# Optimization experiments

Measured on AMD Instinct MI355X. Metric: run time of the kernel, lower is better.

The kernel has to match this reference:

```python
import jax, jax.numpy as jnp
import numpy as np

HID = 4096
NH = 32
NKV = 8
HD = 128
ROPE_BASE = 1000000.0
EPS = 1e-6
Q_SIZE = NH * HD      # 4096
KV_SIZE = NKV * HD    # 1024


def rms_norm(x, w):
    # x: [..., HD]
    var = jnp.mean(x * x, axis=-1, keepdims=True)
    return x * jax.lax.rsqrt(var + EPS) * w


def apply_rope(x, cos, sin):
    # x: [T, H, HD], cos/sin: [T, 1, HD//2]; neox-style rotate-half
    x1, x2 = jnp.split(x, 2, axis=-1)
    return jnp.concatenate([x1 * cos - x2 * sin, x2 * cos + x1 * sin], axis=-1)


def setup_inputs() -> dict:
    key = jax.random.key(0)
    ks = jax.random.split(key, 8)
    T = 4096
    inp = {
        "positions": jnp.arange(T, dtype=jnp.int32),
        "hidden_states": jax.random.normal(ks[0], (T, HID), dtype=jnp.float32),
        "ctx_len": 3072,
        "w_qkv": jax.random.normal(ks[1], (HID, Q_SIZE + 2 * KV_SIZE), dtype=jnp.float32) * 0.02,
        "b_qkv": jax.random.normal(ks[2], (Q_SIZE + 2 * KV_SIZE,), dtype=jnp.float32) * 0.02,
        "q_norm_w": 1.0 + 0.02 * jax.random.normal(ks[3], (HD,), dtype=jnp.float32),
        "k_norm_w": 1.0 + 0.02 * jax.random.normal(ks[4], (HD,), dtype=jnp.float32),
        "w_o": jax.random.normal(ks[5], (Q_SIZE, HID), dtype=jnp.float32) * 0.02,
    }
    return inp


def reference(positions, hidden_states, ctx_len, w_qkv, b_qkv, q_norm_w, k_norm_w, w_o):
    T = hidden_states.shape[0]
    noise_len = T - ctx_len

    qkv = hidden_states @ w_qkv + b_qkv                     # [T, 6144]
    q = qkv[:, :Q_SIZE].reshape(T, NH, HD)
    k = qkv[:, Q_SIZE:Q_SIZE + KV_SIZE].reshape(T, NKV, HD)
    v = qkv[:, Q_SIZE + KV_SIZE:].reshape(T, NKV, HD)

    # per-head RMSNorm on q and k
    q = rms_norm(q, q_norm_w)
    k = rms_norm(k, k_norm_w)

    # RoPE (neox style, full rotary dim)
    half = HD // 2
    inv_freq = 1.0 / (ROPE_BASE ** (jnp.arange(half, dtype=jnp.float32) / half))
    freqs = positions.astype(jnp.float32)[:, None] * inv_freq[None, :]   # [T, half]
    cos = jnp.cos(freqs)[:, None, :]
    sin = jnp.sin(freqs)[:, None, :]
    q = apply_rope(q, cos, sin)
    k = apply_rope(k, cos, sin)

    # Q from noise positions only; K/V from full sequence (non-causal)
    qn = q[ctx_len:]                                        # [N, NH, HD]
    g = NH // NKV
    qn = qn.reshape(noise_len, NKV, g, HD)                  # [N, kv, g, HD]
    scale = HD ** -0.5

    # scores: [kv, g, N, T] in fp32 (faithful to fp32 softmax)
    scores = jnp.einsum("nkgd,tkd->kgnt", qn, k) * scale
    probs = jax.nn.softmax(scores.astype(jnp.float32), axis=-1).astype(v.dtype)
    out = jnp.einsum("kgnt,tkd->nkgd", probs, v)            # [N, kv, g, HD]
    out = out.reshape(noise_len, NH * HD)
    return out @ w_o                                        # [N, HID]
```

## Files before the change

### kernel.cpp

```cpp
#include <hip/hip_runtime.h>
#include <stdint.h>

#define NH 32
#define NKV 8
#define HD 128
#define HID 4096
#define NQKV 6144

typedef __attribute__((ext_vector_type(8))) __bf16 bf16x8;
typedef __attribute__((ext_vector_type(4))) float f32x4;
typedef __attribute__((ext_vector_type(4))) float float4v;
typedef __attribute__((ext_vector_type(8))) unsigned short ushort8v;
typedef __attribute__((ext_vector_type(4))) unsigned short ushort4v;
typedef __attribute__((ext_vector_type(2))) unsigned short ushort2v;

__device__ __forceinline__ unsigned short f2bf(float f) {
  union { float f; unsigned u; } x; x.f = f;
  unsigned r = x.u + 0x7fffu + ((x.u >> 16) & 1u);
  return (unsigned short)(r >> 16);
}

__device__ __forceinline__ void gld16(const void* g, void* l) {
  __builtin_amdgcn_global_load_lds(
      (const __attribute__((address_space(1))) unsigned int*)g,
      (__attribute__((address_space(3))) unsigned int*)l, 16, 0, 0);
}

__device__ __forceinline__ f32x4 mfma16(bf16x8 a, bf16x8 b, f32x4 c) {
  return __builtin_amdgcn_mfma_f32_16x16x32_bf16(a, b, c, 0, 0, 0);
}

__global__ void ropetab(const int* __restrict__ pos, float* __restrict__ cosT,
                        float* __restrict__ sinT) {
  const int t = blockIdx.x, f = threadIdx.x;
  const double inv = exp(-0.2158673524681918 * (double)f);
  const double arg = (double)pos[t] * inv;
  cosT[t * 64 + f] = (float)cos(arg);
  sinT[t * 64 + f] = (float)sin(arg);
}

__global__ void convbf(const float* __restrict__ src, unsigned short* __restrict__ dst,
                       long n4) {
  long i = (long)blockIdx.x * blockDim.x + threadIdx.x;
  const long stride = (long)gridDim.x * blockDim.x;
  for (; i < n4; i += stride) {
    float4v v = *(const float4v*)(src + i * 4);
    ushort4v o;
    o.x = f2bf(v.x); o.y = f2bf(v.y); o.z = f2bf(v.z); o.w = f2bf(v.w);
    *(ushort4v*)(dst + i * 4) = o;
  }
}

__global__ __launch_bounds__(256) void wtrans(const float* __restrict__ W,
                                              unsigned short* __restrict__ Wt,
                                              int K, int N) {
  __shared__ float tile[64][65];
  const int k0 = blockIdx.y * 64, n0 = blockIdx.x * 64;
  const int tid = threadIdx.x;
  const int rk = tid >> 4, cn = (tid & 15) * 4;
#pragma unroll
  for (int rr = 0; rr < 64; rr += 16) {
    float4v v = *(const float4v*)(W + (long)(k0 + rk + rr) * N + n0 + cn);
    tile[rk + rr][cn] = v.x; tile[rk + rr][cn + 1] = v.y;
    tile[rk + rr][cn + 2] = v.z; tile[rk + rr][cn + 3] = v.w;
  }
  __syncthreads();
  const int rn = tid >> 3, ck = (tid & 7) * 8;
#pragma unroll
  for (int rr = 0; rr < 64; rr += 32) {
    ushort8v o;
#pragma unroll
    for (int j = 0; j < 8; ++j) o[j] = f2bf(tile[ck + j][rn + rr]);
    *(ushort8v*)(Wt + (long)(n0 + rn + rr) * K + k0 + ck) = o;
  }
}

__global__ __launch_bounds__(256) void vtrans(const float* __restrict__ qkv,
                                              unsigned short* __restrict__ Vt, int T) {
  __shared__ float tile[64][65];
  const int kvh = blockIdx.z;
  const int t0 = blockIdx.x * 64, d0 = blockIdx.y * 64;
  const int tid = threadIdx.x;
  const int rt = tid >> 4, cd = (tid & 15) * 4;
#pragma unroll
  for (int rr = 0; rr < 64; rr += 16) {
    float4v v = *(const float4v*)(qkv + (long)(t0 + rt + rr) * NQKV + 5120 + kvh * 128 + d0 + cd);
    tile[rt + rr][cd] = v.x; tile[rt + rr][cd + 1] = v.y;
    tile[rt + rr][cd + 2] = v.z; tile[rt + rr][cd + 3] = v.w;
  }
  __syncthreads();
  const int rd = tid >> 3, ct = (tid & 7) * 8;
#pragma unroll
  for (int rr = 0; rr < 64; rr += 32) {
    ushort8v o;
#pragma unroll
    for (int j = 0; j < 8; ++j) o[j] = f2bf(tile[ct + j][rd + rr]);
    *(ushort8v*)(Vt + ((long)kvh * 128 + d0 + rd + rr) * T + t0 + ct) = o;
  }
}

__global__ __launch_bounds__(256) void norm_rope(
    const float* __restrict__ qkv, const float* __restrict__ qw,
    const float* __restrict__ kw, const float* __restrict__ cosT,
    const float* __restrict__ sinT, unsigned short* __restrict__ Qo,
    unsigned short* __restrict__ Ko, int T, int ctx, int noise) {
  const int t = blockIdx.x;
  __shared__ float cs[64], sn[64];
  const int tid = threadIdx.x;
  if (tid < 64) { cs[tid] = cosT[t * 64 + tid]; sn[tid] = sinT[t * 64 + tid]; }
  __syncthreads();
  const int wid = tid >> 6, lane = tid & 63;
  const float* row = qkv + (long)t * NQKV;
  const bool isNoise = (t >= ctx);
  for (int sl = wid; sl < 40; sl += 4) {
    if (sl < 32 && !isNoise) continue;
    const float* x = row + sl * 128;
    float v0 = x[lane * 2], v1 = x[lane * 2 + 1];
    float ss = v0 * v0 + v1 * v1;
#pragma unroll
    for (int off = 32; off >= 1; off >>= 1) ss += __shfl_xor(ss, off);
    const float rinv = rsqrtf(ss * (1.f / 128.f) + 1e-6f);
    const float* w = (sl < 32) ? qw : kw;
    v0 *= rinv * w[lane * 2];
    v1 *= rinv * w[lane * 2 + 1];
    const float p0 = __shfl_xor(v0, 32);
    const float p1 = __shfl_xor(v1, 32);
    const int f0 = (lane * 2) & 63, f1 = (lane * 2 + 1) & 63;
    float o0, o1;
    if (lane < 32) { o0 = v0 * cs[f0] - p0 * sn[f0]; o1 = v1 * cs[f1] - p1 * sn[f1]; }
    else           { o0 = v0 * cs[f0] + p0 * sn[f0]; o1 = v1 * cs[f1] + p1 * sn[f1]; }
    ushort2v o; o.x = f2bf(o0); o.y = f2bf(o1);
    if (sl < 32)
      *(ushort2v*)(Qo + ((long)sl * noise + (t - ctx)) * 128 + lane * 2) = o;
    else
      *(ushort2v*)(Ko + ((long)(sl - 32) * T + t) * 128 + lane * 2) = o;
  }
}

__global__ __launch_bounds__(256) void gemm_bt(
    const unsigned short* __restrict__ A, const unsigned short* __restrict__ Bt,
    float* __restrict__ C, const float* __restrict__ bias, int M, int N, int K) {
  __shared__ unsigned short As[128 * 32];
  __shared__ unsigned short Bs[128 * 32];
  const int tid = threadIdx.x;
  const int wid = tid >> 6, lane = tid & 63;
  const int lr = lane & 15, lg = lane >> 4;
  const long bm = (long)blockIdx.y * 128;
  const long bn = (long)blockIdx.x * 128;
  const int wm = (wid >> 1) * 64;
  const int wn = (wid & 1) * 64;
  const int nz = gridDim.z;
  const int kLen = K / nz;
  const int kOff = blockIdx.z * kLen;
  f32x4 acc[4][4] = {};
  for (int k0 = kOff; k0 < kOff + kLen; k0 += 32) {
#pragma unroll
    for (int c = 0; c < 2; ++c) {
      const int q = c * 4 + wid;
      const int idx = q * 64 + lane;
      const int r = idx >> 2;
      const int ce = (idx & 3) * 8;
      gld16(A + (bm + r) * (long)K + k0 + ce, As + q * 512);
      gld16(Bt + (bn + r) * (long)K + k0 + ce, Bs + q * 512);
    }
    __syncthreads();
    bf16x8 af[4], bfv[4];
#pragma unroll
    for (int i = 0; i < 4; ++i) {
      af[i]  = *(const bf16x8*)(As + (wm + i * 16 + lr) * 32 + lg * 8);
      bfv[i] = *(const bf16x8*)(Bs + (wn + i * 16 + lr) * 32 + lg * 8);
    }
#pragma unroll
    for (int i = 0; i < 4; ++i)
#pragma unroll
      for (int j = 0; j < 4; ++j)
        acc[i][j] = mfma16(af[i], bfv[j], acc[i][j]);
    __syncthreads();
  }
  if (nz == 1) {
#pragma unroll
    for (int i = 0; i < 4; ++i) {
#pragma unroll
      for (int j = 0; j < 4; ++j) {
        const long row = bm + wm + i * 16 + lg * 4;
        const long col = bn + wn + j * 16 + lr;
        const float b = bias ? bias[col] : 0.f;
#pragma unroll
        for (int r = 0; r < 4; ++r)
          C[(row + r) * (long)N + col] = acc[i][j][r] + b;
      }
    }
  } else {
#pragma unroll
    for (int i = 0; i < 4; ++i) {
#pragma unroll
      for (int j = 0; j < 4; ++j) {
        const long row = bm + wm + i * 16 + lg * 4;
        const long col = bn + wn + j * 16 + lr;
#pragma unroll
        for (int r = 0; r < 4; ++r)
          atomicAdd(&C[(row + r) * (long)N + col], acc[i][j][r]);
      }
    }
  }
}

__global__ __launch_bounds__(256) void attn_kernel(
    const unsigned short* __restrict__ Q, const unsigned short* __restrict__ Kb,
    const unsigned short* __restrict__ Vt, unsigned short* __restrict__ Oout,
    int noise, int T, float scale) {
  __shared__ unsigned short Ks[64 * 128];
  __shared__ unsigned short Vs[128 * 64];
  __shared__ unsigned short Ps[4 * 16 * 64];
  const int h = blockIdx.y;
  const int kvh = h >> 2;
  const int tid = threadIdx.x, wid = tid >> 6, lane = tid & 63;
  const int lr = lane & 15, lg = lane >> 4;
  const unsigned short* qb = Q + ((long)h * noise + blockIdx.x * 64 + wid * 16 + lr) * 128;
  bf16x8 qf[4];
#pragma unroll
  for (int kc = 0; kc < 4; ++kc) qf[kc] = *(const bf16x8*)(qb + kc * 32 + lg * 8);
  const unsigned short* kbase = Kb + (long)kvh * T * 128;
  const unsigned short* vbase = Vt + (long)kvh * 128 * T;
  f32x4 accO[8] = {};
  float m_r[4], l_r[4];
#pragma unroll
  for (int r = 0; r < 4; ++r) { m_r[r] = -1e30f; l_r[r] = 0.f; }
  unsigned short* pw = Ps + wid * 1024;
  const int sw = (lr & 7) << 3;
  for (int t0 = 0; t0 < T; t0 += 64) {
#pragma unroll
    for (int c = 0; c < 4; ++c) {
      const int q = c * 4 + wid;
      const int idx = q * 64 + lane;
      const int kgi = (idx & ~7) | ((idx ^ (idx >> 4)) & 7);
      gld16(kbase + (long)t0 * 128 + (long)kgi * 8, Ks + q * 512);
      const int d = idx >> 3;
      const int cg = (idx ^ d) & 7;
      gld16(vbase + (long)d * T + t0 + cg * 8, Vs + q * 512);
    }
    __syncthreads();
    f32x4 s[4] = {};
    __builtin_amdgcn_s_setprio(1);
#pragma unroll
    for (int kc = 0; kc < 4; ++kc)
#pragma unroll
      for (int nt = 0; nt < 4; ++nt) {
        bf16x8 kf = *(const bf16x8*)(Ks + (nt * 16 + lr) * 128 + (((kc * 32) + lg * 8) ^ sw));
        s[nt] = mfma16(qf[kc], kf, s[nt]);
      }
    __builtin_amdgcn_s_setprio(0);
#pragma unroll
    for (int nt = 0; nt < 4; ++nt)
#pragma unroll
      for (int r = 0; r < 4; ++r) s[nt][r] *= scale;
    float mt[4], rs[4];
#pragma unroll
    for (int r = 0; r < 4; ++r)
      mt[r] = fmaxf(fmaxf(s[0][r], s[1][r]), fmaxf(s[2][r], s[3][r]));
#pragma unroll
    for (int off = 8; off >= 1; off >>= 1)
#pragma unroll
      for (int r = 0; r < 4; ++r) mt[r] = fmaxf(mt[r], __shfl_xor(mt[r], off));
    float corr[4];
#pragma unroll
    for (int r = 0; r < 4; ++r) {
      const float mn = fmaxf(m_r[r], mt[r]);
      corr[r] = __expf(m_r[r] - mn);
      m_r[r] = mn;
      rs[r] = 0.f;
    }
#pragma unroll
    for (int nt = 0; nt < 4; ++nt)
#pragma unroll
      for (int r = 0; r < 4; ++r) {
        const float p = __expf(s[nt][r] - m_r[r]);
        s[nt][r] = p;
        rs[r] += p;
      }
#pragma unroll
    for (int off = 8; off >= 1; off >>= 1)
#pragma unroll
      for (int r = 0; r < 4; ++r) rs[r] += __shfl_xor(rs[r], off);
#pragma unroll
    for (int r = 0; r < 4; ++r) l_r[r] = l_r[r] * corr[r] + rs[r];
#pragma unroll
    for (int nd = 0; nd < 8; ++nd)
#pragma unroll
      for (int r = 0; r < 4; ++r) accO[nd][r] *= corr[r];
#pragma unroll
    for (int nt = 0; nt < 4; ++nt)
#pragma unroll
      for (int r = 0; r < 4; ++r) {
        const int prow = lg * 4 + r;
        pw[prow * 64 + ((nt * 16 + lr) ^ ((prow & 7) << 3))] = f2bf(s[nt][r]);
      }
    __syncthreads();
    __builtin_amdgcn_s_setprio(1);
#pragma unroll
    for (int kc = 0; kc < 2; ++kc) {
      bf16x8 pa = *(const bf16x8*)(pw + lr * 64 + (((kc * 32) + lg * 8) ^ sw));
#pragma unroll
      for (int nd = 0; nd < 8; ++nd) {
        bf16x8 vf = *(const bf16x8*)(Vs + (nd * 16 + lr) * 64 + (((kc * 32) + lg * 8) ^ sw));
        accO[nd] = mfma16(pa, vf, accO[nd]);
      }
    }
    __builtin_amdgcn_s_setprio(0);
    __syncthreads();
  }
  float inv[4];
#pragma unroll
  for (int r = 0; r < 4; ++r) inv[r] = 1.f / l_r[r];
  const long orow = (long)blockIdx.x * 64 + wid * 16;
#pragma unroll
  for (int nd = 0; nd < 8; ++nd)
#pragma unroll
    for (int r = 0; r < 4; ++r)
      Oout[(orow + lg * 4 + r) * 4096 + h * 128 + nd * 16 + lr] =
          f2bf(accO[nd][r] * inv[r]);
}

extern "C" void kernel_launch(void* const* d_in, const int* in_sizes, int n_in,
                              void* d_out, int out_size, void* d_ws, size_t ws_size,
                              hipStream_t stream) {
  const int*   positions = (const int*)d_in[0];
  const float* hidden    = (const float*)d_in[1];
  const float* w_qkv     = (const float*)d_in[3];
  const float* b_qkv     = (const float*)d_in[4];
  const float* q_norm_w  = (const float*)d_in[5];
  const float* k_norm_w  = (const float*)d_in[6];
  const float* w_o       = (const float*)d_in[7];
  float* out = (float*)d_out;
  const int T = in_sizes[0];
  const int noise = out_size / HID;
  const int ctx = T - noise;

  char* ws = (char*)d_ws;
  float* qkv_f32 = (float*)ws;
  unsigned short* attn_out = (unsigned short*)ws;
  size_t off = (size_t)T * NQKV * 4;
  unsigned short* Hbf = (unsigned short*)(ws + off);
  unsigned short* WoT = Hbf;
  off += (size_t)T * HID * 2;
  unsigned short* WqkvT = (unsigned short*)(ws + off);
  off += (size_t)NQKV * HID * 2;
  float* cosT = (float*)(ws + off); off += (size_t)T * 64 * 4;
  float* sinT = (float*)(ws + off); off += (size_t)T * 64 * 4;
  unsigned short* Qb  = (unsigned short*)(ws + off); off += (size_t)NH * noise * HD * 2;
  unsigned short* Kbf = (unsigned short*)(ws + off); off += (size_t)NKV * T * HD * 2;
  unsigned short* Vtb = (unsigned short*)(ws + off); off += (size_t)NKV * HD * T * 2;

  ropetab<<<dim3(T), dim3(64), 0, stream>>>(positions, cosT, sinT);
  convbf<<<dim3(2048), dim3(256), 0, stream>>>(hidden, Hbf, (long)T * HID / 4);
  wtrans<<<dim3(NQKV / 64, HID / 64), dim3(256), 0, stream>>>(w_qkv, WqkvT, HID, NQKV);
  gemm_bt<<<dim3(NQKV / 128, T / 128, 1), dim3(256), 0, stream>>>(Hbf, WqkvT, qkv_f32, b_qkv, T, NQKV, HID);
  wtrans<<<dim3(HID / 64, HID / 64), dim3(256), 0, stream>>>(w_o, WoT, HID, HID);
  norm_rope<<<dim3(T), dim3(256), 0, stream>>>(qkv_f32, q_norm_w, k_norm_w, cosT, sinT, Qb, Kbf, T, ctx, noise);
  vtrans<<<dim3(T / 64, HD / 64, NKV), dim3(256), 0, stream>>>(qkv_f32, Vtb, T);
  const float scale = 0.08838834764831845f;
  attn_kernel<<<dim3(noise / 64, NH), dim3(256), 0, stream>>>(Qb, Kbf, Vtb, attn_out, noise, T, scale);
  hipMemsetAsync(d_out, 0, (size_t)out_size * sizeof(float), stream);
  gemm_bt<<<dim3(HID / 128, noise / 128, 2), dim3(256), 0, stream>>>(attn_out, WoT, out, (const float*)nullptr, noise, HID, HID);
}
```

Measured before the change: 803.6 us.

## Skip unused Q projection for context rows, double-buffer GEMMs, replace atomics with split-K reduce

Adds a dedicated QKV GEMM that computes only the K/V columns for context rows and the full Q/K/V columns for noise rows, since Q for context positions is never used. It also adds a block-index swizzle for tile order. Both GEMMs now double-buffer their LDS tiles so the next K-slice load overlaps the MFMA work on the current one. The output projection moves from 2-way split-K with atomicAdd into a memset output to 4-way split-K writing partial buffers, followed by a vectorized reduce kernel. The cost is extra LDS per block and extra global traffic for the partial buffers, which reuse the workspace once held by the qkv scratch.

Result: faster. 643.5 us (-19.9%).

```diff
diff --git a/kernel.cpp b/kernel.cpp
--- a/kernel.cpp
+++ b/kernel.cpp
@@ -137,11 +137,85 @@
   }
 }
 
+__global__ __launch_bounds__(256) void gemm_qkv(
+    const unsigned short* __restrict__ A, const unsigned short* __restrict__ Bt,
+    float* __restrict__ C, const float* __restrict__ bias, int ctx, int nKV) {
+  __shared__ unsigned short As[2][128 * 32];
+  __shared__ unsigned short Bs[2][128 * 32];
+  const int K = HID;
+  const int tid = threadIdx.x;
+  const int wid = tid >> 6, lane = tid & 63;
+  const int lr = lane & 15, lg = lane >> 4;
+  const int cpx = gridDim.x >> 3;
+  const int swz = (blockIdx.x & 7) * cpx + (blockIdx.x >> 3);
+  long bm, bn;
+  if (swz < nKV) {
+    bm = (long)(swz / 16) * 128;
+    bn = 4096 + (long)(swz % 16) * 128;
+  } else {
+    const int r = swz - nKV;
+    bm = ctx + (long)(r / 48) * 128;
+    bn = (long)(r % 48) * 128;
+  }
+  const int wm = (wid >> 1) * 64;
+  const int wn = (wid & 1) * 64;
+  f32x4 acc[4][4] = {};
+
+  const int r0 = (wid * 64 + lane) >> 2;
+  const int ce0 = ((wid * 64 + lane) & 3) * 8;
+  const int r1 = ((4 + wid) * 64 + lane) >> 2;
+  const int ce1 = (((4 + wid) * 64 + lane) & 3) * 8;
+
+#define STAGE(buf, k0)                                                        \
+  do {                                                                        \
+    gld16(A + (bm + r0) * (long)K + (k0) + ce0, As[buf] + wid * 512);         \
+    gld16(Bt + (bn + r0) * (long)K + (k0) + ce0, Bs[buf] + wid * 512);        \
+    gld16(A + (bm + r1) * (long)K + (k0) + ce1, As[buf] + (4 + wid) * 512);   \
+    gld16(Bt + (bn + r1) * (long)K + (k0) + ce1, Bs[buf] + (4 + wid) * 512);  \
+  } while (0)
+
+#define COMPUTE(buf)                                                          \
+  do {                                                                        \
+    bf16x8 af[4], bfv[4];                                                     \
+    _Pragma("unroll") for (int i = 0; i < 4; ++i) {                           \
+      af[i]  = *(const bf16x8*)(As[buf] + (wm + i * 16 + lr) * 32 + lg * 8);  \
+      bfv[i] = *(const bf16x8*)(Bs[buf] + (wn + i * 16 + lr) * 32 + lg * 8);  \
+    }                                                                         \
+    _Pragma("unroll") for (int i = 0; i < 4; ++i)                             \
+      _Pragma("unroll") for (int j = 0; j < 4; ++j)                           \
+        acc[i][j] = mfma16(af[i], bfv[j], acc[i][j]);                         \
+  } while (0)
+
+  STAGE(0, 0);
+  __syncthreads();
+  int cur = 0;
+  for (int k0 = 32; k0 < K; k0 += 32) {
+    STAGE(cur ^ 1, k0);
+    COMPUTE(cur);
+    __syncthreads();
+    cur ^= 1;
+  }
+  COMPUTE(cur);
+
+#pragma unroll
+  for (int i = 0; i < 4; ++i) {
+#pragma unroll
+    for (int j = 0; j < 4; ++j) {
+      const long row = bm + wm + i * 16 + lg * 4;
+      const long col = bn + wn + j * 16 + lr;
+      const float b = bias[col];
+#pragma unroll
+      for (int r = 0; r < 4; ++r)
+        C[(row + r) * (long)NQKV + col] = acc[i][j][r] + b;
+    }
+  }
+}
+
 __global__ __launch_bounds__(256) void gemm_bt(
     const unsigned short* __restrict__ A, const unsigned short* __restrict__ Bt,
-    float* __restrict__ C, const float* __restrict__ bias, int M, int N, int K) {
-  __shared__ unsigned short As[128 * 32];
-  __shared__ unsigned short Bs[128 * 32];
+    float* __restrict__ C, int M, int N, int K) {
+  __shared__ unsigned short As[2][128 * 32];
+  __shared__ unsigned short Bs[2][128 * 32];
   const int tid = threadIdx.x;
   const int wid = tid >> 6, lane = tid & 63;
   const int lr = lane & 15, lg = lane >> 4;
@@ -149,59 +223,51 @@
   const long bn = (long)blockIdx.x * 128;
   const int wm = (wid >> 1) * 64;
   const int wn = (wid & 1) * 64;
-  const int nz = gridDim.z;
-  const int kLen = K / nz;
+  const int kLen = K / gridDim.z;
   const int kOff = blockIdx.z * kLen;
+  float* Cz = C + (size_t)blockIdx.z * M * N;
   f32x4 acc[4][4] = {};
-  for (int k0 = kOff; k0 < kOff + kLen; k0 += 32) {
-#pragma unroll
-    for (int c = 0; c < 2; ++c) {
-      const int q = c * 4 + wid;
-      const int idx = q * 64 + lane;
-      const int r = idx >> 2;
-      const int ce = (idx & 3) * 8;
-      gld16(A + (bm + r) * (long)K + k0 + ce, As + q * 512);
-      gld16(Bt + (bn + r) * (long)K + k0 + ce, Bs + q * 512);
+
+  const int r0 = (wid * 64 + lane) >> 2;
+  const int ce0 = ((wid * 64 + lane) & 3) * 8;
+  const int r1 = ((4 + wid) * 64 + lane) >> 2;
+  const int ce1 = (((4 + wid) * 64 + lane) & 3) * 8;
+
+  STAGE(0, kOff);
+  __syncthreads();
+  int cur = 0;
+  for (int k0 = kOff + 32; k0 < kOff + kLen; k0 += 32) {
+    STAGE(cur ^ 1, k0);
+    COMPUTE(cur);
+    __syncthreads();
+    cur ^= 1;
+  }
+  COMPUTE(cur);
+
+#pragma unroll
+  for (int i = 0; i < 4; ++i) {
+#pragma unroll
+    for (int j = 0; j < 4; ++j) {
+      const long row = bm + wm + i * 16 + lg * 4;
+      const long col = bn + wn + j * 16 + lr;
+#pragma unroll
+      for (int r = 0; r < 4; ++r)
+        Cz[(row + r) * (long)N + col] = acc[i][j][r];
     }
-    __syncthreads();
-    bf16x8 af[4], bfv[4];
-#pragma unroll
-    for (int i = 0; i < 4; ++i) {
-      af[i]  = *(const bf16x8*)(As + (wm + i * 16 + lr) * 32 + lg * 8);
-      bfv[i] = *(const bf16x8*)(Bs + (wn + i * 16 + lr) * 32 + lg * 8);
-    }
-#pragma unroll
-    for (int i = 0; i < 4; ++i)
-#pragma unroll
-      for (int j = 0; j < 4; ++j)
-        acc[i][j] = mfma16(af[i], bfv[j], acc[i][j]);
-    __syncthreads();
-  }
-  if (nz == 1) {
-#pragma unroll
-    for (int i = 0; i < 4; ++i) {
-#pragma unroll
-      for (int j = 0; j < 4; ++j) {
-        const long row = bm + wm + i * 16 + lg * 4;
-        const long col = bn + wn + j * 16 + lr;
-        const float b = bias ? bias[col] : 0.f;
-#pragma unroll
-        for (int r = 0; r < 4; ++r)
-          C[(row + r) * (long)N + col] = acc[i][j][r] + b;
-      }
-    }
-  } else {
-#pragma unroll
-    for (int i = 0; i < 4; ++i) {
-#pragma unroll
-      for (int j = 0; j < 4; ++j) {
-        const long row = bm + wm + i * 16 + lg * 4;
-        const long col = bn + wn + j * 16 + lr;
-#pragma unroll
-        for (int r = 0; r < 4; ++r)
-          atomicAdd(&C[(row + r) * (long)N + col], acc[i][j][r]);
-      }
-    }
+  }
+}
+
+__global__ void reduce4(const float* __restrict__ P, float* __restrict__ out,
+                        long n4, long stride) {
+  long i = (long)blockIdx.x * blockDim.x + threadIdx.x;
+  const long gs = (long)gridDim.x * blockDim.x;
+  for (; i < n4; i += gs) {
+    float4v a = *(const float4v*)(P + i * 4);
+    float4v b = *(const float4v*)(P + stride + i * 4);
+    float4v c = *(const float4v*)(P + 2 * stride + i * 4);
+    float4v d = *(const float4v*)(P + 3 * stride + i * 4);
+    float4v o = a + b + c + d;
+    *(float4v*)(out + i * 4) = o;
   }
 }
 
@@ -339,6 +405,7 @@
   char* ws = (char*)d_ws;
   float* qkv_f32 = (float*)ws;
   unsigned short* attn_out = (unsigned short*)ws;
+  float* Cpart = (float*)(ws + (size_t)16 * 1024 * 1024);
   size_t off = (size_t)T * NQKV * 4;
   unsigned short* Hbf = (unsigned short*)(ws + off);
   unsigned short* WoT = Hbf;
@@ -354,12 +421,14 @@
   ropetab<<<dim3(T), dim3(64), 0, stream>>>(positions, cosT, sinT);
   convbf<<<dim3(2048), dim3(256), 0, stream>>>(hidden, Hbf, (long)T * HID / 4);
   wtrans<<<dim3(NQKV / 64, HID / 64), dim3(256), 0, stream>>>(w_qkv, WqkvT, HID, NQKV);
-  gemm_bt<<<dim3(NQKV / 128, T / 128, 1), dim3(256), 0, stream>>>(Hbf, WqkvT, qkv_f32, b_qkv, T, NQKV, HID);
+  const int nKV = (2048 / 128) * (ctx / 128);
+  const int nNoise = (NQKV / 128) * (noise / 128);
+  gemm_qkv<<<dim3(nKV + nNoise), dim3(256), 0, stream>>>(Hbf, WqkvT, qkv_f32, b_qkv, ctx, nKV);
   wtrans<<<dim3(HID / 64, HID / 64), dim3(256), 0, stream>>>(w_o, WoT, HID, HID);
   norm_rope<<<dim3(T), dim3(256), 0, stream>>>(qkv_f32, q_norm_w, k_norm_w, cosT, sinT, Qb, Kbf, T, ctx, noise);
   vtrans<<<dim3(T / 64, HD / 64, NKV), dim3(256), 0, stream>>>(qkv_f32, Vtb, T);
   const float scale = 0.08838834764831845f;
   attn_kernel<<<dim3(noise / 64, NH), dim3(256), 0, stream>>>(Qb, Kbf, Vtb, attn_out, noise, T, scale);
-  hipMemsetAsync(d_out, 0, (size_t)out_size * sizeof(float), stream);
-  gemm_bt<<<dim3(HID / 128, noise / 128, 2), dim3(256), 0, stream>>>(attn_out, WoT, out, (const float*)nullptr, noise, HID, HID);
-}
+  gemm_bt<<<dim3(HID / 128, noise / 128, 4), dim3(256), 0, stream>>>(attn_out, WoT, Cpart, noise, HID, HID);
+  reduce4<<<dim3(1024), dim3(256), 0, stream>>>(Cpart, out, (long)noise * HID / 4, (long)noise * HID);
+}
```
